# Optimization experiments

Measured on AMD Instinct MI355X. Metric: run time of the kernel, lower is better.

The kernel has to match this reference:

```python
import jax, jax.numpy as jnp
import numpy as np

N_WIRES = 8
DIM = 2 ** N_WIRES  # 256
NUM_HEADS = 4

def _cnot_ring_perm():
    # Compose CNOT(w, w+1) for w=0..6 then CNOT(7, 0) into one basis permutation.
    # Wire 0 is the most-significant bit of the basis index.
    perm = np.arange(DIM)
    pairs = [(w, w + 1) for w in range(N_WIRES - 1)] + [(N_WIRES - 1, 0)]
    j = np.arange(DIM)
    for c, t in pairs:
        ctrl = (j >> (N_WIRES - 1 - c)) & 1
        M = j ^ (ctrl << (N_WIRES - 1 - t))  # flip target bit where control=1 (involution)
        perm = perm[M]
    return perm

PERM = _cnot_ring_perm()
# SIGNS[i, w] = <i|Z_w|i> = 1 - 2*bit_w(i)
SIGNS = np.array([[1.0 - 2.0 * ((i >> (N_WIRES - 1 - w)) & 1) for w in range(N_WIRES)]
                  for i in range(DIM)], dtype=np.float32)

def setup_inputs() -> dict:
    key = jax.random.key(0)
    k1, k2, k3 = jax.random.split(key, 3)
    x = jax.random.normal(k1, (16, 4096, N_WIRES), jnp.float32)  # rotation angles per token
    theta = jax.random.normal(k2, (N_WIRES,), jnp.float32)       # trainable RX params
    w_combine = jax.random.normal(k3, (N_WIRES, N_WIRES), jnp.float32) / np.float32(np.sqrt(N_WIRES))
    b_combine = jnp.zeros((N_WIRES,), jnp.float32)
    return {"x": x, "theta": theta, "w_combine": w_combine, "b_combine": b_combine}

def _quantum_features(x, theta):
    # RX(x_i) then RX(theta_i) on wire i compose to RX(x_i + theta_i) acting on |0>.
    B, S, E = x.shape
    N = B * S
    phi = (x + theta).reshape(N, E)
    c = jnp.cos(0.5 * phi).astype(jnp.complex64)
    s = (-1j) * jnp.sin(0.5 * phi)          # RX|0> = cos(phi/2)|0> - i sin(phi/2)|1>
    wv = jnp.stack([c, s.astype(jnp.complex64)], axis=-1)  # (N, 8, 2)
    # Build product state via successive Kronecker products (wire 0 = MSB).
    state = jnp.ones((N, 1), jnp.complex64)
    for w in range(E):
        state = (state[:, :, None] * wv[:, w, None, :]).reshape(N, -1)  # (N, 2^(w+1))
    state = state[:, jnp.asarray(PERM)]      # apply the CNOT ring as one permutation
    probs = state.real ** 2 + state.imag ** 2  # (N, 256)
    return (probs @ jnp.asarray(SIGNS)).reshape(B, S, E)  # <Z_w> per token

def reference(x, theta, w_combine, b_combine):
    B, S, E = x.shape
    d_k = E // NUM_HEADS
    q = _quantum_features(x, theta)           # (B, S, 8); k = v = q in the source
    scores = jnp.einsum('bse,bte->bst', q, q) / np.float32(np.sqrt(d_k))
    attn = jax.nn.softmax(scores, axis=-1)    # dropout is identity in eval mode
    out = jnp.einsum('bst,bte->bse', attn, q)
    # Faithful to source: transpose(1,2).contiguous().view(B, S, E)
    out = jnp.swapaxes(out, 1, 2).reshape(B, S, E)
    return out @ w_combine.T + b_combine
```

## Files before the change

kernel.cpp:

```cpp
#include <hip/hip_runtime.h>
#include <math.h>


#define SEQ   4096
#define NB    16
#define SROWS 128
#define TPB   1024
#define NTG   4
#define TC    512
#define NCH   (SEQ / TC)
#define TPT   4
#define KSTR  12
#define VSTR  520
#define KFSZ  (TC * KSTR)
#define VTSZ  (9 * VSTR)
#define QTPB  256

typedef _Float16 f16x4  __attribute__((ext_vector_type(4)));
typedef _Float16 f16x8  __attribute__((ext_vector_type(8)));
typedef float    f32x16 __attribute__((ext_vector_type(16)));
typedef __fp16   hf2    __attribute__((ext_vector_type(2)));

#if __has_builtin(__builtin_amdgcn_exp2f)
#define EXP2F(x) __builtin_amdgcn_exp2f(x)
#else
#define EXP2F(x) exp2f(x)
#endif

__global__ __launch_bounds__(QTPB)
void qgen_kernel(const float* __restrict__ x, const float* __restrict__ theta,
                 _Float16* __restrict__ qg, _Float16* __restrict__ qs)
{
    const int n = blockIdx.x * QTPB + threadIdx.x;
    float th[8];
#pragma unroll
    for (int w = 0; w < 8; ++w) th[w] = theta[w];
    const float4 xa  = *(const float4*)(x + (size_t)n * 8);
    const float4 xb4 = *(const float4*)(x + (size_t)n * 8 + 4);
    float c0 = __cosf(xa.x  + th[0]);
    float c1 = __cosf(xa.y  + th[1]);
    float c2 = __cosf(xa.z  + th[2]);
    float c3 = __cosf(xa.w  + th[3]);
    float c4 = __cosf(xb4.x + th[4]);
    float c5 = __cosf(xb4.y + th[5]);
    float c6 = __cosf(xb4.z + th[6]);
    float c7 = __cosf(xb4.w + th[7]);
    float p1 = c0 * c1, p2 = p1 * c2, p3 = p2 * c3, p4 = p3 * c4;
    float p5 = p4 * c5, p6 = p5 * c6, p7 = p6 * c7;
    float p0 = c1 * c2 * c3 * c4 * c5 * c6 * c7;
    const float sc = 0.70710678118654752f * 1.44269504088896341f;
    f16x8 u = (f16x8){(_Float16)p0, (_Float16)p1, (_Float16)p2, (_Float16)p3,
                      (_Float16)p4, (_Float16)p5, (_Float16)p6, (_Float16)p7};
    f16x8 v = (f16x8){(_Float16)(p0*sc), (_Float16)(p1*sc),
                      (_Float16)(p2*sc), (_Float16)(p3*sc),
                      (_Float16)(p4*sc), (_Float16)(p5*sc),
                      (_Float16)(p6*sc), (_Float16)(p7*sc)};
    *(f16x8*)(qg + (size_t)n * 8) = u;
    *(f16x8*)(qs + (size_t)n * 8) = v;
}

__global__ __launch_bounds__(TPB, 8)
void qattn_kernel(const _Float16* __restrict__ qg, const _Float16* __restrict__ qs,
                  const float* __restrict__ wc, const float* __restrict__ bc,
                  float* __restrict__ out)
{
    __shared__ __align__(16) _Float16 kf[2 * KFSZ];
    __shared__ __align__(16) _Float16 vt[2 * VTSZ];
    float* part = (float*)kf;
    float* attn = (float*)vt;

    const int tid  = threadIdx.x;
    const int lane = tid & 63;
    const int wv   = tid >> 6;
    const int sub  = wv & 3;
    const int tg   = wv >> 2;
    const int l31  = lane & 31;
    const int hp   = lane >> 5;

    const int b  = blockIdx.x >> 5;
    const int S0 = (blockIdx.x & 31) * SROWS;
    const _Float16* qbg = qg + (size_t)b * SEQ * 8;

    const int pos = (tid & ~12) | ((tid & 4) << 1) | ((tid & 8) >> 1);

    f16x4 qfrag;
    {
        const int s = S0 + sub * 32 + l31;
        qfrag = *(const f16x4*)(qs + ((size_t)b * SEQ + s) * 8 + 4 * hp);
    }

    auto dswr = [&](int buf, f16x8 h) {
        _Float16* krow = kf + buf * KFSZ + tid * KSTR;
        *(f16x4*)(krow)     = (f16x4){h[0], h[1], h[2], h[3]};
        *(f16x4*)(krow + 4) = (f16x4){h[4], h[5], h[6], h[7]};
        _Float16* vb = vt + buf * VTSZ + pos;
        vb[0 * VSTR] = h[0];
        vb[1 * VSTR] = h[1];
        vb[2 * VSTR] = h[2];
        vb[3 * VSTR] = h[3];
        vb[4 * VSTR] = h[4];
        vb[5 * VSTR] = h[5];
        vb[6 * VSTR] = h[6];
        vb[7 * VSTR] = h[7];
    };

    f16x8 hq;
    if (tid < TC) {
        vt[0 * VTSZ + 8 * VSTR + tid] = (_Float16)1.0f;
        vt[1 * VTSZ + 8 * VSTR + tid] = (_Float16)1.0f;
        dswr(0, *(const f16x8*)(qbg + (size_t)tid * 8));
        hq = *(const f16x8*)(qbg + (size_t)(TC + tid) * 8);
    }

    f32x16 o = {0.f,0.f,0.f,0.f,0.f,0.f,0.f,0.f,0.f,0.f,0.f,0.f,0.f,0.f,0.f,0.f};
    const f32x16 zc = (f32x16){0.f,0.f,0.f,0.f,0.f,0.f,0.f,0.f,
                               0.f,0.f,0.f,0.f,0.f,0.f,0.f,0.f};

    const int wr = (l31 < 8) ? l31 : 8;
    __syncthreads();

    for (int ch = 0; ch < NCH; ++ch) {
        const int c = ch & 1;
        if (ch + 1 < NCH && tid < TC) {
            dswr(c ^ 1, hq);
        }
        if (ch + 2 < NCH && tid < TC) {
            hq = *(const f16x8*)(qbg + (size_t)((ch + 2) * TC + tid) * 8);
        }
        const _Float16* kfb = kf + c * KFSZ + l31 * KSTR + 4 * hp + tg * (TPT * 32) * KSTR;
        const _Float16* vbb = vt + c * VTSZ + wr * VSTR + 8 * hp + tg * (TPT * 32);
#pragma unroll
        for (int i = 0; i < TPT; ++i) {
            f16x4 kfrag = *(const f16x4*)(kfb + i * 32 * KSTR);
            f32x16 cc = __builtin_amdgcn_mfma_f32_32x32x8f16(kfrag, qfrag, zc, 0, 0, 0);
#pragma unroll
            for (int h = 0; h < 2; ++h) {
                union { hf2 q[4]; f16x8 v; } pa;
                pa.q[0] = __builtin_amdgcn_cvt_pkrtz(EXP2F(cc[8*h+0]), EXP2F(cc[8*h+1]));
                pa.q[1] = __builtin_amdgcn_cvt_pkrtz(EXP2F(cc[8*h+2]), EXP2F(cc[8*h+3]));
                pa.q[2] = __builtin_amdgcn_cvt_pkrtz(EXP2F(cc[8*h+4]), EXP2F(cc[8*h+5]));
                pa.q[3] = __builtin_amdgcn_cvt_pkrtz(EXP2F(cc[8*h+6]), EXP2F(cc[8*h+7]));
                f16x8 vfrag = *(const f16x8*)(vbb + i * 32 + h * 16);
                o = __builtin_amdgcn_mfma_f32_32x32x16_f16(pa.v, vfrag, o, 0, 0, 0);
            }
        }
        __syncthreads();
    }

    if (l31 < 9) {
#pragma unroll
        for (int r = 0; r < 16; ++r) {
            const int sloc = sub * 32 + (r & 3) + 8 * (r >> 2) + 4 * hp;
            part[((tg * SROWS) + sloc) * 9 + l31] = o[r];
        }
    }
    __syncthreads();
    for (int idx = tid; idx < SROWS * 9; idx += TPB) {
        const int rr = idx / 9;
        const int w  = idx - rr * 9;
        float sm = 0.f;
#pragma unroll
        for (int g = 0; g < NTG; ++g) sm += part[((g * SROWS) + rr) * 9 + w];
        attn[rr * 9 + w] = sm;
    }
    __syncthreads();
    if (tid < SROWS * 8) {
        const int rr = tid >> 3;
        const int w  = tid & 7;
        attn[rr * 9 + w] = attn[rr * 9 + w] / attn[rr * 9 + 8];
    }
    __syncthreads();

    if (tid < SROWS) {
        const int e    = tid >> 4;
        const int nloc = tid & 15;
        const int r    = e * 512 + (S0 >> 3) + nloc;
        float y[8];
#pragma unroll
        for (int c = 0; c < 8; ++c) y[c] = attn[(nloc * 8 + c) * 9 + e];
        float oo[8];
#pragma unroll
        for (int k = 0; k < 8; ++k) {
            float a = bc[k];
#pragma unroll
            for (int c = 0; c < 8; ++c) a += y[c] * wc[k * 8 + c];
            oo[k] = a;
        }
        float4* op = (float4*)(out + ((size_t)b * SEQ + r) * 8);
        op[0] = make_float4(oo[0], oo[1], oo[2], oo[3]);
        op[1] = make_float4(oo[4], oo[5], oo[6], oo[7]);
    }
}

extern "C" void kernel_launch(void* const* d_in, const int* in_sizes, int n_in,
                              void* d_out, int out_size, void* d_ws, size_t ws_size,
                              hipStream_t stream)
{
    const float* x  = (const float*)d_in[0];
    const float* th = (const float*)d_in[1];
    const float* wc = (const float*)d_in[2];
    const float* bc = (const float*)d_in[3];
    float* out = (float*)d_out;

    _Float16* qg = (_Float16*)d_ws;
    _Float16* qs = qg + (size_t)NB * SEQ * 8;

    qgen_kernel<<<dim3(NB * SEQ / QTPB), dim3(QTPB), 0, stream>>>(x, th, qg, qs);
    qattn_kernel<<<dim3(NB * (SEQ / SROWS)), dim3(TPB), 0, stream>>>(qg, qs, wc, bc, out);
}
```

Baseline: 88.92 us.

## Load K fragments from global memory and double chunk size to 1024

Removes the LDS staging buffer for K and instead has each wave read its K fragments straight from global/L2 memory, with a three-deep rotating register prefetch spread across the tile loop. With the K buffer gone, the chunk size doubles to 1024 tokens per chunk (8 tiles per thread group), so there are half as many chunk iterations and block barriers, and all 1024 threads now fill the V buffer. The intent is to cut LDS write traffic and synchronisation per token. The cost is that global-load latency now sits inside the MFMA loop, and the V buffer, which now also holds the reduction scratch, uses more LDS, which may lower occupancy.

```diff
diff --git a/kernel.cpp b/kernel.cpp
--- a/kernel.cpp
+++ b/kernel.cpp
@@ -7,12 +7,10 @@
 #define SROWS 128
 #define TPB   1024
 #define NTG   4
-#define TC    512
+#define TC    1024
 #define NCH   (SEQ / TC)
-#define TPT   4
-#define KSTR  12
-#define VSTR  520
-#define KFSZ  (TC * KSTR)
+#define TPT   8
+#define VSTR  1032
 #define VTSZ  (9 * VSTR)
 #define QTPB  256
 
@@ -64,10 +62,9 @@
                   const float* __restrict__ wc, const float* __restrict__ bc,
                   float* __restrict__ out)
 {
-    __shared__ __align__(16) _Float16 kf[2 * KFSZ];
     __shared__ __align__(16) _Float16 vt[2 * VTSZ];
-    float* part = (float*)kf;
-    float* attn = (float*)vt;
+    float* part = (float*)vt;
+    float* attn = (float*)(vt + VTSZ);
 
     const int tid  = threadIdx.x;
     const int lane = tid & 63;
@@ -90,9 +87,6 @@
     }
 
     auto dswr = [&](int buf, f16x8 h) {
-        _Float16* krow = kf + buf * KFSZ + tid * KSTR;
-        *(f16x4*)(krow)     = (f16x4){h[0], h[1], h[2], h[3]};
-        *(f16x4*)(krow + 4) = (f16x4){h[4], h[5], h[6], h[7]};
         _Float16* vb = vt + buf * VTSZ + pos;
         vb[0 * VSTR] = h[0];
         vb[1 * VSTR] = h[1];
@@ -105,7 +99,7 @@
     };
 
     f16x8 hq;
-    if (tid < TC) {
+    {
         vt[0 * VTSZ + 8 * VSTR + tid] = (_Float16)1.0f;
         vt[1 * VTSZ + 8 * VSTR + tid] = (_Float16)1.0f;
         dswr(0, *(const f16x8*)(qbg + (size_t)tid * 8));
@@ -121,17 +115,18 @@
 
     for (int ch = 0; ch < NCH; ++ch) {
         const int c = ch & 1;
-        if (ch + 1 < NCH && tid < TC) {
+        if (ch + 1 < NCH) {
             dswr(c ^ 1, hq);
         }
-        if (ch + 2 < NCH && tid < TC) {
+        if (ch + 2 < NCH) {
             hq = *(const f16x8*)(qbg + (size_t)((ch + 2) * TC + tid) * 8);
         }
-        const _Float16* kfb = kf + c * KFSZ + l31 * KSTR + 4 * hp + tg * (TPT * 32) * KSTR;
+        const _Float16* kgb = qbg + (size_t)(ch * TC + tg * (TPT * 32) + l31) * 8 + 4 * hp;
         const _Float16* vbb = vt + c * VTSZ + wr * VSTR + 8 * hp + tg * (TPT * 32);
-#pragma unroll
-        for (int i = 0; i < TPT; ++i) {
-            f16x4 kfrag = *(const f16x4*)(kfb + i * 32 * KSTR);
+        auto KLD = [&](int i) -> f16x4 {
+            return *(const f16x4*)(kgb + (size_t)i * 32 * 8);
+        };
+        auto TILE = [&](f16x4 kfrag, int i) {
             f32x16 cc = __builtin_amdgcn_mfma_f32_32x32x8f16(kfrag, qfrag, zc, 0, 0, 0);
 #pragma unroll
             for (int h = 0; h < 2; ++h) {
@@ -143,7 +138,18 @@
                 f16x8 vfrag = *(const f16x8*)(vbb + i * 32 + h * 16);
                 o = __builtin_amdgcn_mfma_f32_32x32x16_f16(pa.v, vfrag, o, 0, 0, 0);
             }
-        }
+        };
+        f16x4 ka = KLD(0);
+        f16x4 kb = KLD(1);
+        f16x4 kc = KLD(2);
+        TILE(ka, 0); ka = KLD(3);
+        TILE(kb, 1); kb = KLD(4);
+        TILE(kc, 2); kc = KLD(5);
+        TILE(ka, 3); ka = KLD(6);
+        TILE(kb, 4); kb = KLD(7);
+        TILE(kc, 5);
+        TILE(ka, 6);
+        TILE(kb, 7);
         __syncthreads();
     }
 
```

Result: no change. 89.85 us (+1.0%).
